# Kernel tuning notes

Hardware: AMD Instinct MI355X
Metric: run time of the kernel (lower is better)

The kernel has to match this reference:

```python
import jax, jax.numpy as jnp
import numpy as np

DIM = 1024
N_HEADS = 16
HEAD_DIM = DIM // N_HEADS
SCALE = HEAD_DIM ** -0.5


def setup_inputs() -> dict:
    key = jax.random.key(0)
    k1, k2, k3 = jax.random.split(key, 3)
    x = jax.random.normal(k1, (4, 2048, DIM), dtype=jnp.float32)
    w_qkv = jax.random.normal(k2, (DIM, 3 * DIM), dtype=jnp.float32) * (DIM ** -0.5)
    w_proj = jax.random.normal(k3, (DIM, DIM), dtype=jnp.float32) * (DIM ** -0.5)
    b_proj = jnp.zeros((DIM,), dtype=jnp.float32)
    return {"x": x, "w_qkv": w_qkv, "w_proj": w_proj, "b_proj": b_proj}


def reference(x, w_qkv, w_proj, b_proj):
    b, s, d = x.shape
    # qkv projection (no bias), split into q, k, v with per-head layout
    qkv = (x @ w_qkv).reshape(b, s, 3, N_HEADS, HEAD_DIM)
    q, k, v = jnp.moveaxis(qkv, 2, 0)  # each [b, s, h, hd]
    # scaled dot-product attention
    scores = jnp.einsum('bqhd,bkhd->bhqk', q, k) * SCALE
    attn = jax.nn.softmax(scores, axis=-1)
    out = jnp.einsum('bhqk,bkhd->bqhd', attn, v).reshape(b, s, d)
    # output projection (with bias)
    return out @ w_proj + b_proj
```

## Files before the change

kernel.cpp:

```cpp
#include <hip/hip_runtime.h>

#define DIM 1024
#define NHEADS 16
#define HD 64
#define SEQ 2048
#define BATCH 4
#define MROWS (BATCH * SEQ)
#define N3 (3 * DIM)
#define SCALE 0.125f
#define LOG2E 1.4426950408889634f
#define SM_C (SCALE * LOG2E)
#define SMAX 16.0f

typedef __attribute__((ext_vector_type(8))) __bf16 bf16x8;
typedef __attribute__((ext_vector_type(4))) __bf16 bf16x4;
typedef __attribute__((ext_vector_type(4))) float f32x4;

#define MFMA16(a, b, c) __builtin_amdgcn_mfma_f32_16x16x32_bf16((a), (b), (c), 0, 0, 0)

#define GLDS16(g, l)                                                        \
  __builtin_amdgcn_global_load_lds(                                         \
      (const __attribute__((address_space(1))) void*)(g),                   \
      (__attribute__((address_space(3))) void*)(l), 16, 0, 0)

__device__ __forceinline__ unsigned short f2bf(float f) {
  union { float f; unsigned u; } v;
  v.f = f;
  unsigned r = v.u + 0x7fffu + ((v.u >> 16) & 1u);
  return (unsigned short)(r >> 16);
}

__device__ __forceinline__ float exp2_hw(float x) {
  float r;
  asm("v_exp_f32 %0, %1" : "=v"(r) : "v"(x));
  return r;
}


__global__ void cast_x_kernel(const float* __restrict__ x,
                              unsigned short* __restrict__ xb, int n4) {
  int i = blockIdx.x * blockDim.x + threadIdx.x;
  if (i >= n4) return;
  float4 v = ((const float4*)x)[i];
  ushort4 o;
  o.x = f2bf(v.x); o.y = f2bf(v.y); o.z = f2bf(v.z); o.w = f2bf(v.w);
  ((ushort4*)xb)[i] = o;
}

__global__ void tcast_kernel(const float* __restrict__ in,
                             unsigned short* __restrict__ out, int K, int N) {
  __shared__ float tile[32][33];
  int t = threadIdx.x;
  int c = t & 31, r8 = t >> 5;
  int n0 = blockIdx.x * 32, k0 = blockIdx.y * 32;
#pragma unroll
  for (int i = 0; i < 4; ++i) {
    int kr = r8 + i * 8;
    tile[kr][c] = in[(size_t)(k0 + kr) * N + n0 + c];
  }
  __syncthreads();
#pragma unroll
  for (int i = 0; i < 4; ++i) {
    int nr = r8 + i * 8;
    out[(size_t)(n0 + nr) * K + k0 + c] = f2bf(tile[c][nr]);
  }
}


__global__ __launch_bounds__(256, 3)
void gemm_qkv_kernel(const unsigned short* __restrict__ A,
                     const unsigned short* __restrict__ Bt,
                     unsigned short* __restrict__ Qb,
                     unsigned short* __restrict__ Kb,
                     unsigned short* __restrict__ Vt) {
  __shared__ __align__(16) unsigned short As[128 * 64];
  __shared__ __align__(16) unsigned short Bs[128 * 64];
  int t = threadIdx.x;
  int w = t >> 6, l = t & 63;
  int lane16 = l & 15, lhi = l >> 4;
  int mbase = blockIdx.y * 128, nbase = blockIdx.x * 128;
  int wm = (w >> 1) * 64, wn = (w & 1) * 64;

  const int srow = t >> 3;
  const int sslot = (t & 7) ^ ((t >> 3) & 7);
  const unsigned short* Ag = A + (size_t)(mbase + srow) * 1024 + sslot * 8;
  const unsigned short* Bg = Bt + (size_t)(nbase + srow) * 1024 + sslot * 8;

  const int sl0 = ((lhi ^ (lane16 & 7)) << 4);
  const char* Ard = (const char*)As + (wm + lane16) * 128;
  const char* Brd = (const char*)Bs + (wn + lane16) * 128;

  f32x4 acc[4][4];
  f32x4 z4 = {0.f, 0.f, 0.f, 0.f};
#pragma unroll
  for (int i = 0; i < 4; ++i)
#pragma unroll
    for (int j = 0; j < 4; ++j) acc[i][j] = z4;

  for (int kt = 0; kt < 1024; kt += 64) {
#pragma unroll
    for (int i = 0; i < 4; ++i) {
      GLDS16(Ag + (size_t)(i * 32) * 1024 + kt, (char*)As + i * 4096 + w * 1024);
      GLDS16(Bg + (size_t)(i * 32) * 1024 + kt, (char*)Bs + i * 4096 + w * 1024);
    }
    __syncthreads();
#pragma unroll
    for (int kh = 0; kh < 2; ++kh) {
      const int so = sl0 ^ (kh << 6);
      bf16x8 af[4], bfr[4];
#pragma unroll
      for (int mi = 0; mi < 4; ++mi)
        af[mi] = *(const bf16x8*)(Ard + mi * 2048 + so);
#pragma unroll
      for (int ni = 0; ni < 4; ++ni)
        bfr[ni] = *(const bf16x8*)(Brd + ni * 2048 + so);
#pragma unroll
      for (int mi = 0; mi < 4; ++mi)
#pragma unroll
        for (int ni = 0; ni < 4; ++ni)
          acc[mi][ni] = MFMA16(af[mi], bfr[ni], acc[mi][ni]);
    }
    __syncthreads();
  }

#pragma unroll
  for (int mi = 0; mi < 4; ++mi) {
#pragma unroll
    for (int ni = 0; ni < 4; ++ni) {
#pragma unroll
      for (int r = 0; r < 4; ++r) {
        int grow = mbase + wm + mi * 16 + (lhi << 2) + r;
        int gcol = nbase + wn + ni * 16 + lane16;
        int b = grow >> 11, s = grow & 2047;
        unsigned short val = f2bf(acc[mi][ni][r]);
        if (gcol < 1024) {
          int h = gcol >> 6, d = gcol & 63;
          Qb[((size_t)(b * 16 + h) * 2048 + s) * 64 + d] = val;
        } else if (gcol < 2048) {
          int n2 = gcol - 1024;
          int h = n2 >> 6, d = n2 & 63;
          Kb[((size_t)(b * 16 + h) * 2048 + s) * 64 + d] = val;
        } else {
          int n2 = gcol - 2048;
          int h = n2 >> 6, d = n2 & 63;
          Vt[((size_t)(b * 16 + h) * 64 + d) * 2048 + s] = val;
        }
      }
    }
  }
}


__global__ __launch_bounds__(512, 4)
void attn_kernel(const unsigned short* __restrict__ Qb,
                 const unsigned short* __restrict__ Kb,
                 const unsigned short* __restrict__ Vt,
                 unsigned short* __restrict__ attn) {
  __shared__ __align__(16) unsigned short Ks[2][4096];
  __shared__ __align__(16) unsigned short Vs[2][4096];
  __shared__ __align__(16) unsigned short Ps[8][32][72];

  const int t = threadIdx.x, wv = t >> 6, l = t & 63;
  const int lane16 = l & 15, lhi = l >> 4;

  const int bid = blockIdx.x;
  const int nid = (bid & 7) * 64 + (bid >> 3);
  const int qg = nid & 7, h = (nid >> 3) & 15, b = nid >> 7;

  const unsigned short* Qp = Qb + (size_t)(b * NHEADS + h) * SEQ * HD;
  const unsigned short* Kp = Kb + (size_t)(b * NHEADS + h) * SEQ * HD;
  const unsigned short* Vp = Vt + (size_t)(b * NHEADS + h) * HD * SEQ;

  const int q0 = qg * 256 + wv * 32;

  bf16x8 qa[2][2];
#pragma unroll
  for (int mi = 0; mi < 2; ++mi)
#pragma unroll
    for (int kh = 0; kh < 2; ++kh)
      qa[mi][kh] = *(const bf16x8*)(Qp + (size_t)(q0 + mi * 16 + lane16) * HD +
                                    kh * 32 + lhi * 8);

  const int srow = t >> 3;
  const unsigned short* kg = Kp + srow * HD + (((t & 7) ^ ((t >> 5) & 7)) * 8);
  const unsigned short* vg =
      Vp + (size_t)srow * SEQ + (((t & 7) ^ ((t >> 3) & 7)) * 8);

  const int key = lane16 & 7;
  const int off0 = (lhi ^ key) << 4;
  const int off1 = off0 ^ 64;
  const char* krd = (const char*)&Ks[0][0] + lane16 * 512;
  const char* vrd = (const char*)&Vs[0][0] + lane16 * 128;
  unsigned short* pwr = &Ps[wv][0][lane16 * 4];
  const unsigned short* prd = &Ps[wv][lane16][lhi * 8];

  f32x4 z4 = {0.f, 0.f, 0.f, 0.f};
  f32x4 o[2][4];
  float lsum[2][4];
#pragma unroll
  for (int mi = 0; mi < 2; ++mi)
#pragma unroll
    for (int nd = 0; nd < 4; ++nd) o[mi][nd] = z4;
#pragma unroll
  for (int mi = 0; mi < 2; ++mi)
#pragma unroll
    for (int r = 0; r < 4; ++r) lsum[mi][r] = 0.f;

  GLDS16(kg, (char*)&Ks[0][0] + wv * 1024);
  GLDS16(vg, (char*)&Vs[0][0] + wv * 1024);
  __syncthreads();

  int cur = 0;
  for (int ti = 0; ti < SEQ / 64; ++ti) {
    if (ti < SEQ / 64 - 1) {
      const int kb = (ti + 1) * 64;
      GLDS16(kg + (size_t)kb * HD, (char*)&Ks[cur ^ 1][0] + wv * 1024);
      GLDS16(vg + kb, (char*)&Vs[cur ^ 1][0] + wv * 1024);
    }

    const char* kp = krd + cur * 8192;
    bf16x8 kf[4][2];
#pragma unroll
    for (int ni = 0; ni < 4; ++ni) {
      kf[ni][0] = *(const bf16x8*)(kp + ni * 128 + off0);
      kf[ni][1] = *(const bf16x8*)(kp + ni * 128 + off1);
    }
#pragma unroll
    for (int mi = 0; mi < 2; ++mi) {
      f32x4 s[4];
#pragma unroll
      for (int ni = 0; ni < 4; ++ni) {
        f32x4 a = MFMA16(qa[mi][0], kf[ni][0], z4);
        s[ni] = MFMA16(qa[mi][1], kf[ni][1], a);
      }
#pragma unroll
      for (int r = 0; r < 4; ++r) {
        float p0 = exp2_hw(__builtin_fmaf(s[0][r], SM_C, -SMAX));
        float p1 = exp2_hw(__builtin_fmaf(s[1][r], SM_C, -SMAX));
        float p2 = exp2_hw(__builtin_fmaf(s[2][r], SM_C, -SMAX));
        float p3 = exp2_hw(__builtin_fmaf(s[3][r], SM_C, -SMAX));
        lsum[mi][r] += (p0 + p1) + (p2 + p3);
        bf16x4 pk;
        pk[0] = (__bf16)p0; pk[1] = (__bf16)p1;
        pk[2] = (__bf16)p2; pk[3] = (__bf16)p3;
        *(bf16x4*)(pwr + (mi * 16 + (lhi << 2) + r) * 72) = pk;
      }
    }

    bf16x8 pa[2][2];
#pragma unroll
    for (int mi = 0; mi < 2; ++mi)
#pragma unroll
      for (int kvh = 0; kvh < 2; ++kvh)
        pa[mi][kvh] = *(const bf16x8*)(prd + mi * 16 * 72 + kvh * 32);
    const char* vp2 = vrd + cur * 8192;
#pragma unroll
    for (int nd = 0; nd < 4; ++nd) {
      bf16x8 v0 = *(const bf16x8*)(vp2 + nd * 2048 + off0);
      bf16x8 v1 = *(const bf16x8*)(vp2 + nd * 2048 + off1);
#pragma unroll
      for (int mi = 0; mi < 2; ++mi) {
        o[mi][nd] = MFMA16(pa[mi][0], v0, o[mi][nd]);
        o[mi][nd] = MFMA16(pa[mi][1], v1, o[mi][nd]);
      }
    }
    __syncthreads();
    cur ^= 1;
  }

#pragma unroll
  for (int mi = 0; mi < 2; ++mi)
#pragma unroll
    for (int r = 0; r < 4; ++r) {
      float ls = lsum[mi][r];
      ls += __shfl_xor(ls, 1);
      ls += __shfl_xor(ls, 2);
      ls += __shfl_xor(ls, 4);
      ls += __shfl_xor(ls, 8);
      lsum[mi][r] = 1.0f / ls;
    }
  size_t orow_base = (size_t)b * SEQ;
#pragma unroll
  for (int mi = 0; mi < 2; ++mi)
#pragma unroll
    for (int nd = 0; nd < 4; ++nd)
#pragma unroll
      for (int r = 0; r < 4; ++r) {
        int row = q0 + mi * 16 + (lhi << 2) + r;
        attn[(orow_base + row) * DIM + h * HD + nd * 16 + lane16] =
            f2bf(o[mi][nd][r] * lsum[mi][r]);
      }
}


__global__ __launch_bounds__(256, 3)
void gemm_proj_kernel(const unsigned short* __restrict__ A,
                      const unsigned short* __restrict__ Bt,
                      const float* __restrict__ bias,
                      float* __restrict__ out) {
  __shared__ __align__(16) unsigned short As[128 * 64];
  __shared__ __align__(16) unsigned short Bs[128 * 64];
  int t = threadIdx.x;
  int w = t >> 6, l = t & 63;
  int lane16 = l & 15, lhi = l >> 4;
  int mbase = blockIdx.y * 128, nbase = blockIdx.x * 128;
  int wm = (w >> 1) * 64, wn = (w & 1) * 64;

  const int srow = t >> 3;
  const int sslot = (t & 7) ^ ((t >> 3) & 7);
  const unsigned short* Ag = A + (size_t)(mbase + srow) * 1024 + sslot * 8;
  const unsigned short* Bg = Bt + (size_t)(nbase + srow) * 1024 + sslot * 8;

  const int sl0 = ((lhi ^ (lane16 & 7)) << 4);
  const char* Ard = (const char*)As + (wm + lane16) * 128;
  const char* Brd = (const char*)Bs + (wn + lane16) * 128;

  f32x4 acc[4][4];
  f32x4 z4 = {0.f, 0.f, 0.f, 0.f};
#pragma unroll
  for (int i = 0; i < 4; ++i)
#pragma unroll
    for (int j = 0; j < 4; ++j) acc[i][j] = z4;

  for (int kt = 0; kt < 1024; kt += 64) {
#pragma unroll
    for (int i = 0; i < 4; ++i) {
      GLDS16(Ag + (size_t)(i * 32) * 1024 + kt, (char*)As + i * 4096 + w * 1024);
      GLDS16(Bg + (size_t)(i * 32) * 1024 + kt, (char*)Bs + i * 4096 + w * 1024);
    }
    __syncthreads();
#pragma unroll
    for (int kh = 0; kh < 2; ++kh) {
      const int so = sl0 ^ (kh << 6);
      bf16x8 af[4], bfr[4];
#pragma unroll
      for (int mi = 0; mi < 4; ++mi)
        af[mi] = *(const bf16x8*)(Ard + mi * 2048 + so);
#pragma unroll
      for (int ni = 0; ni < 4; ++ni)
        bfr[ni] = *(const bf16x8*)(Brd + ni * 2048 + so);
#pragma unroll
      for (int mi = 0; mi < 4; ++mi)
#pragma unroll
        for (int ni = 0; ni < 4; ++ni)
          acc[mi][ni] = MFMA16(af[mi], bfr[ni], acc[mi][ni]);
    }
    __syncthreads();
  }

#pragma unroll
  for (int mi = 0; mi < 4; ++mi) {
#pragma unroll
    for (int ni = 0; ni < 4; ++ni) {
#pragma unroll
      for (int r = 0; r < 4; ++r) {
        int grow = mbase + wm + mi * 16 + (lhi << 2) + r;
        int gcol = nbase + wn + ni * 16 + lane16;
        out[(size_t)grow * 1024 + gcol] = acc[mi][ni][r] + bias[gcol];
      }
    }
  }
}


extern "C" void kernel_launch(void* const* d_in, const int* in_sizes, int n_in,
                              void* d_out, int out_size, void* d_ws,
                              size_t ws_size, hipStream_t stream) {
  const float* x = (const float*)d_in[0];
  const float* w_qkv = (const float*)d_in[1];
  const float* w_proj = (const float*)d_in[2];
  const float* b_proj = (const float*)d_in[3];
  float* out = (float*)d_out;
  char* ws = (char*)d_ws;

  unsigned short* xb = (unsigned short*)(ws);
  unsigned short* attnb = (unsigned short*)(ws);
  unsigned short* wqkvT = (unsigned short*)(ws + (16ull << 20));
  unsigned short* wprojT = (unsigned short*)(ws + (22ull << 20));
  unsigned short* Qb = (unsigned short*)(ws + (24ull << 20));
  unsigned short* Kb = (unsigned short*)(ws + (40ull << 20));
  unsigned short* Vt = (unsigned short*)(ws + (56ull << 20));

  int n4 = MROWS * DIM / 4;
  cast_x_kernel<<<n4 / 256, 256, 0, stream>>>(x, xb, n4);
  tcast_kernel<<<dim3(N3 / 32, DIM / 32), 256, 0, stream>>>(w_qkv, wqkvT, DIM, N3);
  tcast_kernel<<<dim3(DIM / 32, DIM / 32), 256, 0, stream>>>(w_proj, wprojT, DIM, DIM);
  gemm_qkv_kernel<<<dim3(N3 / 128, MROWS / 128), 256, 0, stream>>>(xb, wqkvT, Qb, Kb, Vt);
  attn_kernel<<<512, 512, 0, stream>>>(Qb, Kb, Vt, attnb);
  gemm_proj_kernel<<<dim3(DIM / 128, MROWS / 128), 256, 0, stream>>>(attnb, wprojT, b_proj, out);
}
```

Before: 206.9 us.

## Rewrite QKV GEMM as 256x256 double-buffered tile with XCD-aware block remap

The QKV projection GEMM moves from 128x128 tiles with 4 waves and a single LDS buffer to 256x256 tiles with 8 waves. LDS is now double-buffered, so global-to-LDS loads for the next k-step are issued during the current step's MFMAs. The k-step is split into four phases with explicit barriers and priority boosts, and a block-index remap spreads neighbouring tiles across XCDs to improve L2 reuse. The larger register footprint (8x4 accumulators) and 128KB of LDS limit occupancy, and the hand-placed waits and barriers add correctness risk.

```diff
diff --git a/kernel.cpp b/kernel.cpp
--- a/kernel.cpp
+++ b/kernel.cpp
@@ -23,6 +23,8 @@
       (const __attribute__((address_space(1))) void*)(g),                   \
       (__attribute__((address_space(3))) void*)(l), 16, 0, 0)
 
+#define VMWAIT(N) asm volatile("s_waitcnt vmcnt(" #N ")" ::: "memory")
+
 __device__ __forceinline__ unsigned short f2bf(float f) {
   union { float f; unsigned u; } v;
   v.f = f;
@@ -67,72 +69,121 @@
 }
 
 
-__global__ __launch_bounds__(256, 3)
+#define STAGE_A(H, KT, NB) do {                                              \
+    GLDS16(Ag + (size_t)((H) * 128) * 1024 + (KT),                           \
+           (char*)As + (NB) * 32768 + (H) * 16384 + t * 16);                 \
+    GLDS16(Ag + (size_t)((H) * 128 + 64) * 1024 + (KT),                      \
+           (char*)As + (NB) * 32768 + (H) * 16384 + 8192 + t * 16);          \
+  } while (0)
+
+#define STAGE_B(H, KT, NB) do {                                              \
+    GLDS16(Bg + (size_t)((H) * 128) * 1024 + (KT),                           \
+           (char*)Bs + (NB) * 32768 + (H) * 16384 + t * 16);                 \
+    GLDS16(Bg + (size_t)((H) * 128 + 64) * 1024 + (KT),                      \
+           (char*)Bs + (NB) * 32768 + (H) * 16384 + 8192 + t * 16);          \
+  } while (0)
+
+#define STAGE_TILE(KT, NB) do {                                              \
+    STAGE_A(0, KT, NB); STAGE_A(1, KT, NB);                                  \
+    STAGE_B(0, KT, NB); STAGE_B(1, KT, NB);                                  \
+  } while (0)
+
+#define PHASE(MH, NH, STAGE_STMT, WAIT_STMT) do {                            \
+    bf16x8 af[4][2], bfr[2][2];                                              \
+    const char* ab = Abuf + (wm + (MH) * 64 + lane16) * 128;                 \
+    const char* bb = Bbuf + (wn + (NH) * 32 + lane16) * 128;                 \
+    _Pragma("unroll") for (int i = 0; i < 4; ++i) {                          \
+      af[i][0] = *(const bf16x8*)(ab + i * 2048 + ((lhi << 4) ^ key4));      \
+      af[i][1] = *(const bf16x8*)(ab + i * 2048 + (((lhi | 4) << 4) ^ key4));\
+    }                                                                        \
+    _Pragma("unroll") for (int j = 0; j < 2; ++j) {                          \
+      bfr[j][0] = *(const bf16x8*)(bb + j * 2048 + ((lhi << 4) ^ key4));     \
+      bfr[j][1] = *(const bf16x8*)(bb + j * 2048 + (((lhi | 4) << 4) ^ key4));\
+    }                                                                        \
+    STAGE_STMT;                                                              \
+    WAIT_STMT;                                                               \
+    __builtin_amdgcn_s_barrier();                                            \
+    asm volatile("s_waitcnt lgkmcnt(0)" ::: "memory");                       \
+    __builtin_amdgcn_sched_barrier(0);                                       \
+    __builtin_amdgcn_s_setprio(1);                                           \
+    _Pragma("unroll") for (int i = 0; i < 4; ++i)                            \
+      _Pragma("unroll") for (int j = 0; j < 2; ++j) {                        \
+        acc[(MH)*4+i][(NH)*2+j] =                                            \
+            MFMA16(af[i][0], bfr[j][0], acc[(MH)*4+i][(NH)*2+j]);            \
+        acc[(MH)*4+i][(NH)*2+j] =                                            \
+            MFMA16(af[i][1], bfr[j][1], acc[(MH)*4+i][(NH)*2+j]);            \
+      }                                                                      \
+    __builtin_amdgcn_s_setprio(0);                                           \
+    __builtin_amdgcn_s_barrier();                                            \
+  } while (0)
+
+__global__ __launch_bounds__(512, 2)
 void gemm_qkv_kernel(const unsigned short* __restrict__ A,
                      const unsigned short* __restrict__ Bt,
                      unsigned short* __restrict__ Qb,
                      unsigned short* __restrict__ Kb,
                      unsigned short* __restrict__ Vt) {
-  __shared__ __align__(16) unsigned short As[128 * 64];
-  __shared__ __align__(16) unsigned short Bs[128 * 64];
-  int t = threadIdx.x;
-  int w = t >> 6, l = t & 63;
-  int lane16 = l & 15, lhi = l >> 4;
-  int mbase = blockIdx.y * 128, nbase = blockIdx.x * 128;
-  int wm = (w >> 1) * 64, wn = (w & 1) * 64;
+  __shared__ __align__(16) unsigned short As[2][16384];
+  __shared__ __align__(16) unsigned short Bs[2][16384];
+  const int t = threadIdx.x;
+  const int wv = t >> 6, l = t & 63;
+  const int lane16 = l & 15, lhi = l >> 4;
+
+  const int lin = blockIdx.x;
+  const int nid = (lin & 7) * 48 + (lin >> 3);
+  const int by = nid / 12, bx = nid % 12;
+  const int mbase = by * 256, nbase = bx * 256;
+
+  const int wm = (wv >> 2) * 128;
+  const int wn = (wv & 3) * 64;
 
   const int srow = t >> 3;
-  const int sslot = (t & 7) ^ ((t >> 3) & 7);
-  const unsigned short* Ag = A + (size_t)(mbase + srow) * 1024 + sslot * 8;
-  const unsigned short* Bg = Bt + (size_t)(nbase + srow) * 1024 + sslot * 8;
-
-  const int sl0 = ((lhi ^ (lane16 & 7)) << 4);
-  const char* Ard = (const char*)As + (wm + lane16) * 128;
-  const char* Brd = (const char*)Bs + (wn + lane16) * 128;
-
-  f32x4 acc[4][4];
+  const int scol = ((t & 7) ^ ((t >> 3) & 7)) * 8;
+  const unsigned short* Ag = A + (size_t)(mbase + srow) * 1024 + scol;
+  const unsigned short* Bg = Bt + (size_t)(nbase + srow) * 1024 + scol;
+
+  const int key4 = (lane16 & 7) << 4;
+
+  f32x4 acc[8][4];
   f32x4 z4 = {0.f, 0.f, 0.f, 0.f};
 #pragma unroll
-  for (int i = 0; i < 4; ++i)
+  for (int i = 0; i < 8; ++i)
 #pragma unroll
     for (int j = 0; j < 4; ++j) acc[i][j] = z4;
 
-  for (int kt = 0; kt < 1024; kt += 64) {
-#pragma unroll
-    for (int i = 0; i < 4; ++i) {
-      GLDS16(Ag + (size_t)(i * 32) * 1024 + kt, (char*)As + i * 4096 + w * 1024);
-      GLDS16(Bg + (size_t)(i * 32) * 1024 + kt, (char*)Bs + i * 4096 + w * 1024);
-    }
-    __syncthreads();
-#pragma unroll
-    for (int kh = 0; kh < 2; ++kh) {
-      const int so = sl0 ^ (kh << 6);
-      bf16x8 af[4], bfr[4];
-#pragma unroll
-      for (int mi = 0; mi < 4; ++mi)
-        af[mi] = *(const bf16x8*)(Ard + mi * 2048 + so);
-#pragma unroll
-      for (int ni = 0; ni < 4; ++ni)
-        bfr[ni] = *(const bf16x8*)(Brd + ni * 2048 + so);
-#pragma unroll
-      for (int mi = 0; mi < 4; ++mi)
-#pragma unroll
-        for (int ni = 0; ni < 4; ++ni)
-          acc[mi][ni] = MFMA16(af[mi], bfr[ni], acc[mi][ni]);
-    }
-    __syncthreads();
-  }
-
-#pragma unroll
-  for (int mi = 0; mi < 4; ++mi) {
-#pragma unroll
-    for (int ni = 0; ni < 4; ++ni) {
+  STAGE_TILE(0, 0);
+  VMWAIT(0);
+  __builtin_amdgcn_s_barrier();
+
+  for (int tk = 0; tk < 15; ++tk) {
+    const int buf = tk & 1, nb2 = buf ^ 1;
+    const int ktn = (tk + 1) << 6;
+    const char* Abuf = (const char*)As + buf * 32768;
+    const char* Bbuf = (const char*)Bs + buf * 32768;
+    PHASE(0, 0, STAGE_TILE(ktn, nb2), (void)0);
+    PHASE(1, 0, (void)0, (void)0);
+    PHASE(1, 1, (void)0, (void)0);
+    PHASE(0, 1, (void)0, VMWAIT(0));
+  }
+  {
+    const char* Abuf = (const char*)As + 32768;
+    const char* Bbuf = (const char*)Bs + 32768;
+    PHASE(0, 0, (void)0, (void)0);
+    PHASE(1, 0, (void)0, (void)0);
+    PHASE(1, 1, (void)0, (void)0);
+    PHASE(0, 1, (void)0, (void)0);
+  }
+
+#pragma unroll
+  for (int mf = 0; mf < 8; ++mf) {
+#pragma unroll
+    for (int nf = 0; nf < 4; ++nf) {
 #pragma unroll
       for (int r = 0; r < 4; ++r) {
-        int grow = mbase + wm + mi * 16 + (lhi << 2) + r;
-        int gcol = nbase + wn + ni * 16 + lane16;
+        int grow = mbase + wm + mf * 16 + (lhi << 2) + r;
+        int gcol = nbase + wn + nf * 16 + lane16;
         int b = grow >> 11, s = grow & 2047;
-        unsigned short val = f2bf(acc[mi][ni][r]);
+        unsigned short val = f2bf(acc[mf][nf][r]);
         if (gcol < 1024) {
           int h = gcol >> 6, d = gcol & 63;
           Qb[((size_t)(b * 16 + h) * 2048 + s) * 64 + d] = val;
@@ -298,8 +349,8 @@
                       const unsigned short* __restrict__ Bt,
                       const float* __restrict__ bias,
                       float* __restrict__ out) {
-  __shared__ __align__(16) unsigned short As[128 * 64];
-  __shared__ __align__(16) unsigned short Bs[128 * 64];
+  __shared__ __align__(16) unsigned short Asp[128 * 64];
+  __shared__ __align__(16) unsigned short Bsp[128 * 64];
   int t = threadIdx.x;
   int w = t >> 6, l = t & 63;
   int lane16 = l & 15, lhi = l >> 4;
@@ -312,8 +363,8 @@
   const unsigned short* Bg = Bt + (size_t)(nbase + srow) * 1024 + sslot * 8;
 
   const int sl0 = ((lhi ^ (lane16 & 7)) << 4);
-  const char* Ard = (const char*)As + (wm + lane16) * 128;
-  const char* Brd = (const char*)Bs + (wn + lane16) * 128;
+  const char* Ard = (const char*)Asp + (wm + lane16) * 128;
+  const char* Brd = (const char*)Bsp + (wn + lane16) * 128;
 
   f32x4 acc[4][4];
   f32x4 z4 = {0.f, 0.f, 0.f, 0.f};
@@ -325,8 +376,8 @@
   for (int kt = 0; kt < 1024; kt += 64) {
 #pragma unroll
     for (int i = 0; i < 4; ++i) {
-      GLDS16(Ag + (size_t)(i * 32) * 1024 + kt, (char*)As + i * 4096 + w * 1024);
-      GLDS16(Bg + (size_t)(i * 32) * 1024 + kt, (char*)Bs + i * 4096 + w * 1024);
+      GLDS16(Ag + (size_t)(i * 32) * 1024 + kt, (char*)Asp + i * 4096 + w * 1024);
+      GLDS16(Bg + (size_t)(i * 32) * 1024 + kt, (char*)Bsp + i * 4096 + w * 1024);
     }
     __syncthreads();
 #pragma unroll
@@ -385,7 +436,7 @@
   cast_x_kernel<<<n4 / 256, 256, 0, stream>>>(x, xb, n4);
   tcast_kernel<<<dim3(N3 / 32, DIM / 32), 256, 0, stream>>>(w_qkv, wqkvT, DIM, N3);
   tcast_kernel<<<dim3(DIM / 32, DIM / 32), 256, 0, stream>>>(w_proj, wprojT, DIM, DIM);
-  gemm_qkv_kernel<<<dim3(N3 / 128, MROWS / 128), 256, 0, stream>>>(xb, wqkvT, Qb, Kb, Vt);
+  gemm_qkv_kernel<<<384, 512, 0, stream>>>(xb, wqkvT, Qb, Kb, Vt);
   attn_kernel<<<512, 512, 0, stream>>>(Qb, Kb, Vt, attnb);
   gemm_proj_kernel<<<dim3(DIM / 128, MROWS / 128), 256, 0, stream>>>(attnb, wprojT, b_proj, out);
 }
```

New measurement: 227.7 us. +10.0%, slower.
